# Performance work log

Hardware: AMD Instinct MI355X
Metric: run time of the kernel (lower is better)

Reference implementation:

```python
import jax, jax.numpy as jnp
import numpy as np

B, S, D, H = 2, 2048, 1024, 16
DH = D // H


def setup_inputs() -> dict:
    key = jax.random.key(0)
    ks = jax.random.split(key, 12)
    s = 1.0 / np.sqrt(D)
    inp = {
        "query": jax.random.normal(ks[0], (B, S, D), jnp.float32),
        "key": jax.random.normal(ks[1], (B, S, D), jnp.float32),
        "value": jax.random.normal(ks[2], (B, S, D), jnp.float32),
        "Wq": jax.random.uniform(ks[3], (D, D), jnp.float32, -s, s),
        "bq": jax.random.uniform(ks[4], (D,), jnp.float32, -s, s),
        "Wk": jax.random.uniform(ks[5], (D, D), jnp.float32, -s, s),
        "bk": jax.random.uniform(ks[6], (D,), jnp.float32, -s, s),
        "Wv": jax.random.uniform(ks[7], (D, D), jnp.float32, -s, s),
        "bv": jax.random.uniform(ks[8], (D,), jnp.float32, -s, s),
        "Wo": jax.random.uniform(ks[9], (D, D), jnp.float32, -s, s),
        "bo": jax.random.uniform(ks[10], (D,), jnp.float32, -s, s),
    }
    return inp


def reference(query, key, value, Wq, bq, Wk, bk, Wv, bv, Wo, bo):
    # q,k,v: [B,S,D] -> [B,H,S,Dh]
    def split_heads(x):
        return x.reshape(B, S, H, DH).transpose(0, 2, 1, 3)

    q = split_heads(query @ Wq.T + bq)
    k = split_heads(key @ Wk.T + bk)
    v = split_heads(value @ Wv.T + bv)
    scale = 1.0 / jnp.sqrt(jnp.float32(DH))
    scores = jnp.einsum("bhqd,bhkd->bhqk", q, k) * scale  # [B,H,S,S]
    attn = jax.nn.softmax(scores, axis=-1)
    # dropout is identity in eval mode
    out = jnp.einsum("bhqk,bhkd->bhqd", attn, v)  # [B,H,S,Dh]
    out = out.transpose(0, 2, 1, 3).reshape(B, S, D)
    out = out @ Wo.T + bo
    return out, attn
```

## Files before the change

kernel.cpp:

```cpp
#include <hip/hip_runtime.h>

#define SS 2048

typedef __attribute__((ext_vector_type(4))) float floatx4;
typedef __attribute__((ext_vector_type(8))) __bf16 bf16x8;

__device__ inline unsigned short f2bf(float f) {
  union { float f; unsigned u; } x; x.f = f;
  unsigned r = x.u + 0x7fffu + ((x.u >> 16) & 1u);
  return (unsigned short)(r >> 16);
}

__global__ __launch_bounds__(256) void gemm_proj(
    const float* __restrict__ X, const float* __restrict__ W,
    const float* __restrict__ bias, void* __restrict__ outp, int mode)
{
  __shared__ unsigned short lA[128][40];
  __shared__ unsigned short lB[128][40];
  const int t = threadIdx.x;
  const int nb = blockIdx.x, mb = blockIdx.y;
  const int lane = t & 63, w = t >> 6;
  const int lr = lane & 15, lq = lane >> 4;
  const int wm = w >> 1, wn = w & 1;

  floatx4 acc[4][4];
  for (int j = 0; j < 4; ++j) {
    float bj = bias[nb * 128 + wn * 64 + j * 16 + lr];
    floatx4 bj4 = {bj, bj, bj, bj};
    for (int i = 0; i < 4; ++i) acc[i][j] = bj4;
  }

  for (int kc = 0; kc < 32; ++kc) {
    for (int i = 0; i < 4; ++i) {
      int idx = t + i * 256;
      int row = idx >> 3, c4 = idx & 7;
      const float4 va = *(const float4*)&X[(size_t)(mb * 128 + row) * 1024 + kc * 32 + c4 * 4];
      *(ushort4*)&lA[row][c4 * 4] =
          make_ushort4(f2bf(va.x), f2bf(va.y), f2bf(va.z), f2bf(va.w));
      const float4 vb = *(const float4*)&W[(size_t)(nb * 128 + row) * 1024 + kc * 32 + c4 * 4];
      *(ushort4*)&lB[row][c4 * 4] =
          make_ushort4(f2bf(vb.x), f2bf(vb.y), f2bf(vb.z), f2bf(vb.w));
    }
    __syncthreads();
    bf16x8 aF[4], bF[4];
    for (int i = 0; i < 4; ++i)
      aF[i] = *(const bf16x8*)&lA[wm * 64 + i * 16 + lr][lq * 8];
    for (int j = 0; j < 4; ++j)
      bF[j] = *(const bf16x8*)&lB[wn * 64 + j * 16 + lr][lq * 8];
    for (int i = 0; i < 4; ++i)
      for (int j = 0; j < 4; ++j)
        acc[i][j] = __builtin_amdgcn_mfma_f32_16x16x32_bf16(aF[i], bF[j], acc[i][j], 0, 0, 0);
    __syncthreads();
  }

  if (mode == 2) {
    float* O = (float*)outp;
    for (int i = 0; i < 4; ++i) {
      int m0 = mb * 128 + wm * 64 + i * 16 + lq * 4;
      for (int j = 0; j < 4; ++j) {
        int n = nb * 128 + wn * 64 + j * 16 + lr;
        for (int r = 0; r < 4; ++r)
          O[(size_t)(m0 + r) * 1024 + n] = acc[i][j][r];
      }
    }
  } else if (mode == 0) {
    unsigned short* O = (unsigned short*)outp;
    for (int i = 0; i < 4; ++i) {
      int m0 = mb * 128 + wm * 64 + i * 16 + lq * 4;
      for (int j = 0; j < 4; ++j) {
        int n = nb * 128 + wn * 64 + j * 16 + lr;
        int h = n >> 6, dh = n & 63;
        for (int r = 0; r < 4; ++r) {
          int m = m0 + r;
          int b = m >> 11, s = m & 2047;
          O[((size_t)(b * 16 + h) * 2048 + s) * 64 + dh] = f2bf(acc[i][j][r]);
        }
      }
    }
  } else {
    unsigned short* O = (unsigned short*)outp;
    for (int i = 0; i < 4; ++i) {
      int m0 = mb * 128 + wm * 64 + i * 16 + lq * 4;
      int b = m0 >> 11, s0 = m0 & 2047;
      for (int j = 0; j < 4; ++j) {
        int n = nb * 128 + wn * 64 + j * 16 + lr;
        int h = n >> 6, dh = n & 63;
        *(ushort4*)&O[((size_t)(b * 16 + h) * 64 + dh) * 2048 + s0] =
            make_ushort4(f2bf(acc[i][j][0]), f2bf(acc[i][j][1]),
                         f2bf(acc[i][j][2]), f2bf(acc[i][j][3]));
      }
    }
  }
}

__global__ __launch_bounds__(256) void attn_kernel(
    const unsigned short* __restrict__ Q, const unsigned short* __restrict__ K,
    const unsigned short* __restrict__ Vt, float* __restrict__ attn,
    float* __restrict__ ctx)
{
  __shared__ unsigned short pt[4][32][72];
  const int t = threadIdx.x;
  const int w = t >> 6, lane = t & 63;
  const int lr = lane & 15, lq = lane >> 4;
  const int gw = blockIdx.x * 4 + w;
  const int bh = gw >> 6;
  const int q0 = (gw & 63) * 32;
  const int b = bh >> 4, h = bh & 15;

  const unsigned short* qp = Q + (size_t)bh * SS * 64;
  const unsigned short* kp = K + (size_t)bh * SS * 64;
  const unsigned short* vp = Vt + (size_t)bh * 64 * SS;
  float* aout = attn + (size_t)bh * SS * SS;

  bf16x8 qF[2][2];
  for (int mt = 0; mt < 2; ++mt)
    for (int kk = 0; kk < 2; ++kk)
      qF[mt][kk] = *(const bf16x8*)&qp[(size_t)(q0 + mt * 16 + lr) * 64 + kk * 32 + lq * 8];

  const floatx4 zf = {0.f, 0.f, 0.f, 0.f};
  float lsum[2][4] = {{0.f, 0.f, 0.f, 0.f}, {0.f, 0.f, 0.f, 0.f}};

  for (int kc = 0; kc < 32; ++kc) {
    for (int nt = 0; nt < 4; ++nt) {
      const size_t kbase = (size_t)(kc * 64 + nt * 16 + lr) * 64 + lq * 8;
      bf16x8 kF0 = *(const bf16x8*)&kp[kbase];
      bf16x8 kF1 = *(const bf16x8*)&kp[kbase + 32];
      for (int mt = 0; mt < 2; ++mt) {
        floatx4 s = __builtin_amdgcn_mfma_f32_16x16x32_bf16(qF[mt][0], kF0, zf, 0, 0, 0);
        s = __builtin_amdgcn_mfma_f32_16x16x32_bf16(qF[mt][1], kF1, s, 0, 0, 0);
        for (int r = 0; r < 4; ++r)
          lsum[mt][r] += __expf(s[r] * 0.125f);
      }
    }
  }
  float rl[2][4];
  for (int mt = 0; mt < 2; ++mt)
    for (int r = 0; r < 4; ++r) {
      float v = lsum[mt][r];
      v += __shfl_xor(v, 1);
      v += __shfl_xor(v, 2);
      v += __shfl_xor(v, 4);
      v += __shfl_xor(v, 8);
      rl[mt][r] = 1.0f / v;
    }

  floatx4 oF[2][4];
  for (int mt = 0; mt < 2; ++mt)
    for (int nt = 0; nt < 4; ++nt) oF[mt][nt] = zf;

  for (int kc = 0; kc < 32; ++kc) {
    for (int nt = 0; nt < 4; ++nt) {
      const size_t kbase = (size_t)(kc * 64 + nt * 16 + lr) * 64 + lq * 8;
      bf16x8 kF0 = *(const bf16x8*)&kp[kbase];
      bf16x8 kF1 = *(const bf16x8*)&kp[kbase + 32];
      for (int mt = 0; mt < 2; ++mt) {
        floatx4 s = __builtin_amdgcn_mfma_f32_16x16x32_bf16(qF[mt][0], kF0, zf, 0, 0, 0);
        s = __builtin_amdgcn_mfma_f32_16x16x32_bf16(qF[mt][1], kF1, s, 0, 0, 0);
        for (int r = 0; r < 4; ++r) {
          float p = __expf(s[r] * 0.125f) * rl[mt][r];
          int row = mt * 16 + lq * 4 + r;
          aout[(size_t)(q0 + row) * 2048 + kc * 64 + nt * 16 + lr] = p;
          pt[w][row][nt * 16 + lr] = f2bf(p);
        }
      }
    }
    for (int kk = 0; kk < 2; ++kk) {
      bf16x8 aP[2];
      for (int mt = 0; mt < 2; ++mt)
        aP[mt] = *(const bf16x8*)&pt[w][mt * 16 + lr][kk * 32 + lq * 8];
      for (int nt = 0; nt < 4; ++nt) {
        bf16x8 vF = *(const bf16x8*)&vp[(size_t)(nt * 16 + lr) * 2048 + kc * 64 + kk * 32 + lq * 8];
        for (int mt = 0; mt < 2; ++mt)
          oF[mt][nt] = __builtin_amdgcn_mfma_f32_16x16x32_bf16(aP[mt], vF, oF[mt][nt], 0, 0, 0);
      }
    }
  }

  for (int mt = 0; mt < 2; ++mt)
    for (int nt = 0; nt < 4; ++nt)
      for (int r = 0; r < 4; ++r) {
        int row = q0 + mt * 16 + lq * 4 + r;
        int col = h * 64 + nt * 16 + lr;
        ctx[(size_t)(b * 2048 + row) * 1024 + col] = oF[mt][nt][r];
      }
}

extern "C" void kernel_launch(void* const* d_in, const int* in_sizes, int n_in,
                              void* d_out, int out_size, void* d_ws, size_t ws_size,
                              hipStream_t stream) {
  (void)in_sizes; (void)n_in; (void)out_size; (void)ws_size;
  const float* query = (const float*)d_in[0];
  const float* key   = (const float*)d_in[1];
  const float* value = (const float*)d_in[2];
  const float* Wq = (const float*)d_in[3];
  const float* bq = (const float*)d_in[4];
  const float* Wk = (const float*)d_in[5];
  const float* bk = (const float*)d_in[6];
  const float* Wv = (const float*)d_in[7];
  const float* bv = (const float*)d_in[8];
  const float* Wo = (const float*)d_in[9];
  const float* bo = (const float*)d_in[10];
  float* outF = (float*)d_out;

  unsigned short* q_s = (unsigned short*)d_ws;
  unsigned short* k_s = q_s + 4194304;
  unsigned short* v_t = k_s + 4194304;
  float* ctx = (float*)(v_t + 4194304);

  dim3 gg(8, 32), bb(256);
  gemm_proj<<<gg, bb, 0, stream>>>(query, Wq, bq, (void*)q_s, 0);
  gemm_proj<<<gg, bb, 0, stream>>>(key,   Wk, bk, (void*)k_s, 0);
  gemm_proj<<<gg, bb, 0, stream>>>(value, Wv, bv, (void*)v_t, 1);
  attn_kernel<<<dim3(512), bb, 0, stream>>>(q_s, k_s, v_t, outF + 4194304, ctx);
  gemm_proj<<<gg, bb, 0, stream>>>(ctx, Wo, bo, (void*)outF, 2);
}
```

Measured before the change: 1.086 ms.

## Pre-convert inputs to bf16, batch QKV GEMMs, retile attention with coalesced stores

A new kernel converts the activations and all weights to bf16 in one pass. The three QKV projections then run as a single batched launch with a 64-wide K-chunk that copies bf16 straight into LDS, without per-tile conversion. The attention kernel moves from 32 to 16 query rows per wave, doubling the grid, and uses a swizzled block order. It stages probabilities in an fp32 LDS tile so the attention matrix is written with coalesced float4 stores, and it writes the context in bf16 to halve that traffic. The cost is an extra conversion pass over the inputs and K/V being reloaded twice as often per query row.

```diff
diff --git a/kernel.cpp b/kernel.cpp
--- a/kernel.cpp
+++ b/kernel.cpp
@@ -4,6 +4,7 @@
 
 typedef __attribute__((ext_vector_type(4))) float floatx4;
 typedef __attribute__((ext_vector_type(8))) __bf16 bf16x8;
+typedef __attribute__((ext_vector_type(8))) unsigned short ushortx8;
 
 __device__ inline unsigned short f2bf(float f) {
   union { float f; unsigned u; } x; x.f = f;
@@ -11,12 +12,33 @@
   return (unsigned short)(r >> 16);
 }
 
-__global__ __launch_bounds__(256) void gemm_proj(
-    const float* __restrict__ X, const float* __restrict__ W,
+__global__ __launch_bounds__(256) void cvt_bf16(
+    const float* __restrict__ q, const float* __restrict__ k,
+    const float* __restrict__ v, const float* __restrict__ wq,
+    const float* __restrict__ wk, const float* __restrict__ wv,
+    const float* __restrict__ wo, unsigned short* __restrict__ dst)
+{
+  const size_t f = ((size_t)blockIdx.x * 256 + threadIdx.x) * 4;
+  const float* src;
+  if (f < 4194304) src = q + f;
+  else if (f < 8388608) src = k + (f - 4194304);
+  else if (f < 12582912) src = v + (f - 8388608);
+  else {
+    size_t off = f - 12582912;
+    unsigned wi = (unsigned)(off >> 20);
+    const float* wp = wi == 0 ? wq : wi == 1 ? wk : wi == 2 ? wv : wo;
+    src = wp + (off & 1048575);
+  }
+  float4 x = *(const float4*)src;
+  *(ushort4*)&dst[f] = make_ushort4(f2bf(x.x), f2bf(x.y), f2bf(x.z), f2bf(x.w));
+}
+
+__device__ __forceinline__ void gemm_body(
+    const unsigned short* __restrict__ X, const unsigned short* __restrict__ W,
     const float* __restrict__ bias, void* __restrict__ outp, int mode)
 {
-  __shared__ unsigned short lA[128][40];
-  __shared__ unsigned short lB[128][40];
+  __shared__ unsigned short lA[128][72];
+  __shared__ unsigned short lB[128][72];
   const int t = threadIdx.x;
   const int nb = blockIdx.x, mb = blockIdx.y;
   const int lane = t & 63, w = t >> 6;
@@ -30,26 +52,26 @@
     for (int i = 0; i < 4; ++i) acc[i][j] = bj4;
   }
 
-  for (int kc = 0; kc < 32; ++kc) {
+  for (int kc = 0; kc < 16; ++kc) {
     for (int i = 0; i < 4; ++i) {
       int idx = t + i * 256;
-      int row = idx >> 3, c4 = idx & 7;
-      const float4 va = *(const float4*)&X[(size_t)(mb * 128 + row) * 1024 + kc * 32 + c4 * 4];
-      *(ushort4*)&lA[row][c4 * 4] =
-          make_ushort4(f2bf(va.x), f2bf(va.y), f2bf(va.z), f2bf(va.w));
-      const float4 vb = *(const float4*)&W[(size_t)(nb * 128 + row) * 1024 + kc * 32 + c4 * 4];
-      *(ushort4*)&lB[row][c4 * 4] =
-          make_ushort4(f2bf(vb.x), f2bf(vb.y), f2bf(vb.z), f2bf(vb.w));
+      int row = idx >> 3, c = idx & 7;
+      *(uint4*)&lA[row][c * 8] =
+          *(const uint4*)&X[(size_t)(mb * 128 + row) * 1024 + kc * 64 + c * 8];
+      *(uint4*)&lB[row][c * 8] =
+          *(const uint4*)&W[(size_t)(nb * 128 + row) * 1024 + kc * 64 + c * 8];
     }
     __syncthreads();
-    bf16x8 aF[4], bF[4];
-    for (int i = 0; i < 4; ++i)
-      aF[i] = *(const bf16x8*)&lA[wm * 64 + i * 16 + lr][lq * 8];
-    for (int j = 0; j < 4; ++j)
-      bF[j] = *(const bf16x8*)&lB[wn * 64 + j * 16 + lr][lq * 8];
-    for (int i = 0; i < 4; ++i)
+    for (int kk = 0; kk < 2; ++kk) {
+      bf16x8 aF[4], bF[4];
+      for (int i = 0; i < 4; ++i)
+        aF[i] = *(const bf16x8*)&lA[wm * 64 + i * 16 + lr][kk * 32 + lq * 8];
       for (int j = 0; j < 4; ++j)
-        acc[i][j] = __builtin_amdgcn_mfma_f32_16x16x32_bf16(aF[i], bF[j], acc[i][j], 0, 0, 0);
+        bF[j] = *(const bf16x8*)&lB[wn * 64 + j * 16 + lr][kk * 32 + lq * 8];
+      for (int i = 0; i < 4; ++i)
+        for (int j = 0; j < 4; ++j)
+          acc[i][j] = __builtin_amdgcn_mfma_f32_16x16x32_bf16(aF[i], bF[j], acc[i][j], 0, 0, 0);
+    }
     __syncthreads();
   }
 
@@ -93,18 +115,41 @@
   }
 }
 
+__global__ __launch_bounds__(256) void gemm_qkv(
+    const unsigned short* __restrict__ base, const float* __restrict__ bq,
+    const float* __restrict__ bk, const float* __restrict__ bv,
+    unsigned short* __restrict__ q_s, unsigned short* __restrict__ k_s,
+    unsigned short* __restrict__ v_t)
+{
+  const int z = blockIdx.z;
+  const unsigned short* X = base + (size_t)z * 4194304;
+  const unsigned short* W = base + 12582912 + (size_t)z * 1048576;
+  const float* bias = z == 0 ? bq : z == 1 ? bk : bv;
+  void* out = z == 0 ? (void*)q_s : z == 1 ? (void*)k_s : (void*)v_t;
+  gemm_body(X, W, bias, out, z == 2 ? 1 : 0);
+}
+
+__global__ __launch_bounds__(256) void gemm_out(
+    const unsigned short* __restrict__ ctxb, const unsigned short* __restrict__ Wob,
+    const float* __restrict__ bo, float* __restrict__ out)
+{
+  gemm_body(ctxb, Wob, bo, (void*)out, 2);
+}
+
 __global__ __launch_bounds__(256) void attn_kernel(
     const unsigned short* __restrict__ Q, const unsigned short* __restrict__ K,
     const unsigned short* __restrict__ Vt, float* __restrict__ attn,
-    float* __restrict__ ctx)
-{
-  __shared__ unsigned short pt[4][32][72];
+    unsigned short* __restrict__ ctxb)
+{
+  __shared__ float pf[4][16][68];
   const int t = threadIdx.x;
   const int w = t >> 6, lane = t & 63;
   const int lr = lane & 15, lq = lane >> 4;
-  const int gw = blockIdx.x * 4 + w;
-  const int bh = gw >> 6;
-  const int q0 = (gw & 63) * 32;
+  const int bid = blockIdx.x;
+  const int vb = ((bid & 7) << 7) | (bid >> 3);
+  const int gw = vb * 4 + w;
+  const int bh = gw >> 7;
+  const int q0 = (gw & 127) * 16;
   const int b = bh >> 4, h = bh & 15;
 
   const unsigned short* qp = Q + (size_t)bh * SS * 64;
@@ -112,77 +157,76 @@
   const unsigned short* vp = Vt + (size_t)bh * 64 * SS;
   float* aout = attn + (size_t)bh * SS * SS;
 
-  bf16x8 qF[2][2];
-  for (int mt = 0; mt < 2; ++mt)
-    for (int kk = 0; kk < 2; ++kk)
-      qF[mt][kk] = *(const bf16x8*)&qp[(size_t)(q0 + mt * 16 + lr) * 64 + kk * 32 + lq * 8];
+  bf16x8 qF[2];
+  for (int kk = 0; kk < 2; ++kk)
+    qF[kk] = *(const bf16x8*)&qp[(size_t)(q0 + lr) * 64 + kk * 32 + lq * 8];
 
   const floatx4 zf = {0.f, 0.f, 0.f, 0.f};
-  float lsum[2][4] = {{0.f, 0.f, 0.f, 0.f}, {0.f, 0.f, 0.f, 0.f}};
+  float lsum[4] = {0.f, 0.f, 0.f, 0.f};
 
   for (int kc = 0; kc < 32; ++kc) {
     for (int nt = 0; nt < 4; ++nt) {
       const size_t kbase = (size_t)(kc * 64 + nt * 16 + lr) * 64 + lq * 8;
       bf16x8 kF0 = *(const bf16x8*)&kp[kbase];
       bf16x8 kF1 = *(const bf16x8*)&kp[kbase + 32];
-      for (int mt = 0; mt < 2; ++mt) {
-        floatx4 s = __builtin_amdgcn_mfma_f32_16x16x32_bf16(qF[mt][0], kF0, zf, 0, 0, 0);
-        s = __builtin_amdgcn_mfma_f32_16x16x32_bf16(qF[mt][1], kF1, s, 0, 0, 0);
-        for (int r = 0; r < 4; ++r)
-          lsum[mt][r] += __expf(s[r] * 0.125f);
-      }
-    }
-  }
-  float rl[2][4];
-  for (int mt = 0; mt < 2; ++mt)
-    for (int r = 0; r < 4; ++r) {
-      float v = lsum[mt][r];
-      v += __shfl_xor(v, 1);
-      v += __shfl_xor(v, 2);
-      v += __shfl_xor(v, 4);
-      v += __shfl_xor(v, 8);
-      rl[mt][r] = 1.0f / v;
-    }
-
-  floatx4 oF[2][4];
-  for (int mt = 0; mt < 2; ++mt)
-    for (int nt = 0; nt < 4; ++nt) oF[mt][nt] = zf;
+      floatx4 s = __builtin_amdgcn_mfma_f32_16x16x32_bf16(qF[0], kF0, zf, 0, 0, 0);
+      s = __builtin_amdgcn_mfma_f32_16x16x32_bf16(qF[1], kF1, s, 0, 0, 0);
+      for (int r = 0; r < 4; ++r)
+        lsum[r] += __expf(s[r] * 0.125f);
+    }
+  }
+  float rl[4];
+  for (int r = 0; r < 4; ++r) {
+    float v = lsum[r];
+    v += __shfl_xor(v, 1);
+    v += __shfl_xor(v, 2);
+    v += __shfl_xor(v, 4);
+    v += __shfl_xor(v, 8);
+    rl[r] = 1.0f / v;
+  }
+
+  floatx4 oF[4];
+  for (int nt = 0; nt < 4; ++nt) oF[nt] = zf;
 
   for (int kc = 0; kc < 32; ++kc) {
     for (int nt = 0; nt < 4; ++nt) {
       const size_t kbase = (size_t)(kc * 64 + nt * 16 + lr) * 64 + lq * 8;
       bf16x8 kF0 = *(const bf16x8*)&kp[kbase];
       bf16x8 kF1 = *(const bf16x8*)&kp[kbase + 32];
-      for (int mt = 0; mt < 2; ++mt) {
-        floatx4 s = __builtin_amdgcn_mfma_f32_16x16x32_bf16(qF[mt][0], kF0, zf, 0, 0, 0);
-        s = __builtin_amdgcn_mfma_f32_16x16x32_bf16(qF[mt][1], kF1, s, 0, 0, 0);
-        for (int r = 0; r < 4; ++r) {
-          float p = __expf(s[r] * 0.125f) * rl[mt][r];
-          int row = mt * 16 + lq * 4 + r;
-          aout[(size_t)(q0 + row) * 2048 + kc * 64 + nt * 16 + lr] = p;
-          pt[w][row][nt * 16 + lr] = f2bf(p);
-        }
+      floatx4 s = __builtin_amdgcn_mfma_f32_16x16x32_bf16(qF[0], kF0, zf, 0, 0, 0);
+      s = __builtin_amdgcn_mfma_f32_16x16x32_bf16(qF[1], kF1, s, 0, 0, 0);
+      for (int r = 0; r < 4; ++r)
+        pf[w][lq * 4 + r][nt * 16 + lr] = __expf(s[r] * 0.125f) * rl[r];
+    }
+    {
+      const int sc = lane & 15, sr = lane >> 4;
+      for (int i = 0; i < 4; ++i) {
+        float4 v4 = *(const float4*)&pf[w][sr + i * 4][sc * 4];
+        *(float4*)&aout[(size_t)(q0 + sr + i * 4) * 2048 + kc * 64 + sc * 4] = v4;
       }
     }
     for (int kk = 0; kk < 2; ++kk) {
-      bf16x8 aP[2];
-      for (int mt = 0; mt < 2; ++mt)
-        aP[mt] = *(const bf16x8*)&pt[w][mt * 16 + lr][kk * 32 + lq * 8];
+      const float* pr = &pf[w][lr][kk * 32 + lq * 8];
+      float4 p0 = *(const float4*)pr;
+      float4 p1 = *(const float4*)(pr + 4);
+      union { ushortx8 u; bf16x8 b; } ap;
+      ap.u[0] = f2bf(p0.x); ap.u[1] = f2bf(p0.y);
+      ap.u[2] = f2bf(p0.z); ap.u[3] = f2bf(p0.w);
+      ap.u[4] = f2bf(p1.x); ap.u[5] = f2bf(p1.y);
+      ap.u[6] = f2bf(p1.z); ap.u[7] = f2bf(p1.w);
       for (int nt = 0; nt < 4; ++nt) {
         bf16x8 vF = *(const bf16x8*)&vp[(size_t)(nt * 16 + lr) * 2048 + kc * 64 + kk * 32 + lq * 8];
-        for (int mt = 0; mt < 2; ++mt)
-          oF[mt][nt] = __builtin_amdgcn_mfma_f32_16x16x32_bf16(aP[mt], vF, oF[mt][nt], 0, 0, 0);
-      }
-    }
-  }
-
-  for (int mt = 0; mt < 2; ++mt)
-    for (int nt = 0; nt < 4; ++nt)
-      for (int r = 0; r < 4; ++r) {
-        int row = q0 + mt * 16 + lq * 4 + r;
-        int col = h * 64 + nt * 16 + lr;
-        ctx[(size_t)(b * 2048 + row) * 1024 + col] = oF[mt][nt][r];
-      }
+        oF[nt] = __builtin_amdgcn_mfma_f32_16x16x32_bf16(ap.b, vF, oF[nt], 0, 0, 0);
+      }
+    }
+  }
+
+  for (int nt = 0; nt < 4; ++nt)
+    for (int r = 0; r < 4; ++r) {
+      int row = q0 + lq * 4 + r;
+      int col = h * 64 + nt * 16 + lr;
+      ctxb[(size_t)(b * 2048 + row) * 1024 + col] = f2bf(oF[nt][r]);
+    }
 }
 
 extern "C" void kernel_launch(void* const* d_in, const int* in_sizes, int n_in,
@@ -202,15 +246,14 @@
   const float* bo = (const float*)d_in[10];
   float* outF = (float*)d_out;
 
-  unsigned short* q_s = (unsigned short*)d_ws;
+  unsigned short* cw  = (unsigned short*)d_ws;
+  unsigned short* q_s = cw + 16777216;
   unsigned short* k_s = q_s + 4194304;
   unsigned short* v_t = k_s + 4194304;
-  float* ctx = (float*)(v_t + 4194304);
-
-  dim3 gg(8, 32), bb(256);
-  gemm_proj<<<gg, bb, 0, stream>>>(query, Wq, bq, (void*)q_s, 0);
-  gemm_proj<<<gg, bb, 0, stream>>>(key,   Wk, bk, (void*)k_s, 0);
-  gemm_proj<<<gg, bb, 0, stream>>>(value, Wv, bv, (void*)v_t, 1);
-  attn_kernel<<<dim3(512), bb, 0, stream>>>(q_s, k_s, v_t, outF + 4194304, ctx);
-  gemm_proj<<<gg, bb, 0, stream>>>(ctx, Wo, bo, (void*)outF, 2);
-}
+  unsigned short* ctxb = v_t + 4194304;
+
+  cvt_bf16<<<dim3(16384), dim3(256), 0, stream>>>(query, key, value, Wq, Wk, Wv, Wo, cw);
+  gemm_qkv<<<dim3(8, 32, 3), dim3(256), 0, stream>>>(cw, bq, bk, bv, q_s, k_s, v_t);
+  attn_kernel<<<dim3(1024), dim3(256), 0, stream>>>(q_s, k_s, v_t, outF + 4194304, ctxb);
+  gemm_out<<<dim3(8, 32), dim3(256), 0, stream>>>(ctxb, cw + 15728640, bo, outF);
+}
```

Result: faster. 960.3 us (-11.6%).
